# Performance work log

Hardware: AMD Instinct MI355X
Metric: run time of the kernel (lower is better)

Reference implementation:

```python
import jax, jax.numpy as jnp
import numpy as np

N_NODES = 100000


def _mean_agg(x, src, dst, n_nodes):
    # gather neighbor (src) features, segment-sum into destination nodes, divide by in-degree
    summed = jax.ops.segment_sum(x[src], dst, num_segments=n_nodes)  # [N, d]
    deg = jax.ops.segment_sum(jnp.ones_like(dst, dtype=x.dtype), dst, num_segments=n_nodes)
    return summed / jnp.clip(deg, 1.0)[:, None]  # DGL clamps zero in-degree to 1


def _sage_conv(x, src, dst, W_self, W_neigh, b, n_nodes):
    h_neigh = _mean_agg(x, src, dst, n_nodes)
    # DGL SAGEConv(mean): fc_self(h_self) + fc_neigh(h_neigh); single bias
    return x @ W_self + h_neigh @ W_neigh + b


def setup_inputs() -> dict:
    key = jax.random.key(0)
    ks = jax.random.split(key, 8)
    in_f, hid_f, out_f = 64, 64, 16
    n_edges = 1200000
    return {
        "x": jax.random.normal(ks[0], (N_NODES, in_f), dtype=jnp.float32),
        "src": jax.random.randint(ks[1], (n_edges,), 0, N_NODES),
        "dst": jax.random.randint(ks[2], (n_edges,), 0, N_NODES),
        "W1_self": jax.random.normal(ks[3], (in_f, hid_f), dtype=jnp.float32) / np.sqrt(in_f),
        "W1_neigh": jax.random.normal(ks[4], (in_f, hid_f), dtype=jnp.float32) / np.sqrt(in_f),
        "b1": jnp.zeros((hid_f,), dtype=jnp.float32),
        "W2_self": jax.random.normal(ks[5], (hid_f, out_f), dtype=jnp.float32) / np.sqrt(hid_f),
        "W2_neigh": jax.random.normal(ks[6], (hid_f, out_f), dtype=jnp.float32) / np.sqrt(hid_f),
        "b2": jnp.zeros((out_f,), dtype=jnp.float32),
    }


def reference(x, src, dst, W1_self, W1_neigh, b1, W2_self, W2_neigh, b2):
    h = _sage_conv(x, src, dst, W1_self, W1_neigh, b1, N_NODES)
    h = jax.nn.relu(h)
    h = _sage_conv(h, src, dst, W2_self, W2_neigh, b2, N_NODES)
    return h
```

## Files before the change

### kernel.cpp

```cpp
#include <hip/hip_runtime.h>

#define N_NODES 100000
#define N_EDGES 1200000
#define BK 64
#define NB 1563
#define CHUNK_E 4096
#define NBLK_E 293
#define TOT_H (NB * NBLK_E)
#define NSB2 ((TOT_H + 1023) / 1024)
#define CAP 1536
#define ND1 3125

#define OFF_ROWPTR 0
#define OFF_HISTG  401408
#define OFF_BLK2   2234368
#define OFF_PAIRS  2236416
#define OFF_SORTED 7036928
#define OFF_Y1     11837440
#define OFF_H1     24637440

__device__ __forceinline__ unsigned short f2bf(float f) {
    unsigned u = __float_as_uint(f);
    unsigned r = (u + 0x7fffu + ((u >> 16) & 1u)) >> 16;
    return (unsigned short)r;
}

__global__ __launch_bounds__(256) void hist_dense1_kernel(
    const int* __restrict__ dst, int* __restrict__ hist_g,
    const float* __restrict__ x,
    const float* __restrict__ Wn, const float* __restrict__ Ws,
    const float* __restrict__ b,
    unsigned short* __restrict__ y1, float* __restrict__ z1)
{
    __shared__ float sx[32 * 64];
    const int t = threadIdx.x;

    if (blockIdx.x < NBLK_E) {
        int* h = (int*)sx;
        const int e0 = blockIdx.x * CHUNK_E;
        const int e1 = min(e0 + CHUNK_E, N_EDGES);
        for (int i = t; i < NB; i += 256) h[i] = 0;
        __syncthreads();
        for (int e = e0 + t; e < e1; e += 256)
            atomicAdd(&h[dst[e] >> 6], 1);
        __syncthreads();
        for (int i = t; i < NB; i += 256)
            hist_g[i * NBLK_E + blockIdx.x] = h[i];
        return;
    }

    const int bid = blockIdx.x - NBLK_E;
    const int w = t >> 6;
    const int lane = t & 63;
    const int half = w >> 1;
    const int nsub = (w & 1) * 16;
    const int chunk = bid * 32;

    {
        const float4* gx = (const float4*)(x + (size_t)chunk * 64);
        float4* sx4 = (float4*)sx;
        sx4[t] = gx[t];
        sx4[t + 256] = gx[t + 256];
    }

    const float* W = half ? Ws : Wn;
    float wr[64];
#pragma unroll
    for (int k = 0; k < 64; ++k) wr[k] = W[k * 64 + lane];
    const float bj = half ? b[lane] : 0.f;

    __syncthreads();

#pragma unroll 2
    for (int m = 0; m < 16; ++m) {
        const int node = nsub + m;
        const float4* xr = (const float4*)(sx + node * 64);
        float a0 = 0.f, a1 = 0.f, a2 = 0.f, a3 = 0.f;
#pragma unroll
        for (int k4 = 0; k4 < 16; ++k4) {
            float4 v = xr[k4];
            a0 += v.x * wr[4 * k4 + 0];
            a1 += v.y * wr[4 * k4 + 1];
            a2 += v.z * wr[4 * k4 + 2];
            a3 += v.w * wr[4 * k4 + 3];
        }
        const float o = (a0 + a1) + (a2 + a3) + bj;
        const size_t gn = (size_t)(chunk + node);
        if (half) z1[gn * 64 + lane] = o;
        else      y1[gn * 64 + lane] = f2bf(o);
    }
}

__global__ __launch_bounds__(1024) void scan2_blocks_kernel(
    int* __restrict__ hist_g, int* __restrict__ blk2)
{
    __shared__ int wsum[16];
    const int t = threadIdx.x;
    const int i = blockIdx.x * 1024 + t;
    const int v = (i < TOT_H) ? hist_g[i] : 0;
    int inc = v;
#pragma unroll
    for (int off = 1; off < 64; off <<= 1) {
        int n = __shfl_up(inc, off);
        if ((t & 63) >= off) inc += n;
    }
    const int wid = t >> 6;
    if ((t & 63) == 63) wsum[wid] = inc;
    __syncthreads();
    if (t < 16) {
        int s = wsum[t];
#pragma unroll
        for (int off = 1; off < 16; off <<= 1) {
            int n = __shfl_up(s, off);
            if (t >= off) s += n;
        }
        wsum[t] = s;
    }
    __syncthreads();
    const int base = (wid > 0) ? wsum[wid - 1] : 0;
    const int incl = inc + base;
    if (i < TOT_H) hist_g[i] = incl - v;
    if (t == 1023) blk2[blockIdx.x] = incl;
}

__global__ __launch_bounds__(512) void tops_scan_kernel(int* __restrict__ blk2)
{
    __shared__ int wsum[8];
    const int t = threadIdx.x;
    const int v = (t < NSB2) ? blk2[t] : 0;
    int inc = v;
#pragma unroll
    for (int off = 1; off < 64; off <<= 1) {
        int n = __shfl_up(inc, off);
        if ((t & 63) >= off) inc += n;
    }
    const int wid = t >> 6;
    if ((t & 63) == 63) wsum[wid] = inc;
    __syncthreads();
    if (t < 8) {
        int s = wsum[t];
#pragma unroll
        for (int off = 1; off < 8; off <<= 1) {
            int n = __shfl_up(s, off);
            if (t >= off) s += n;
        }
        wsum[t] = s;
    }
    __syncthreads();
    const int base = (wid > 0) ? wsum[wid - 1] : 0;
    if (t < NSB2) blk2[t] = inc + base - v;
}

__global__ __launch_bounds__(512) void pair_scatter_kernel(
    const int* __restrict__ src, const int* __restrict__ dst,
    const int* __restrict__ hs_scan, const int* __restrict__ blk2,
    unsigned* __restrict__ pairs)
{
    __shared__ int base_s[NB];
    __shared__ int cur_s[NB];
    const int b = blockIdx.x;
    const int t = threadIdx.x;
    const int e0 = b * CHUNK_E;
    const int e1 = min(e0 + CHUNK_E, N_EDGES);

    for (int i = t; i < NB; i += 512) {
        int idx = i * NBLK_E + b;
        base_s[i] = hs_scan[idx] + blk2[idx >> 10];
        cur_s[i] = 0;
    }
    __syncthreads();
    for (int e = e0 + t; e < e1; e += 512) {
        int d = dst[e];
        int bk = d >> 6;
        int pos = base_s[bk] + atomicAdd(&cur_s[bk], 1);
        pairs[pos] = ((unsigned)src[e] << 6) | (unsigned)(d & 63);
    }
}

__global__ __launch_bounds__(512) void fused_gather1_kernel(
    const unsigned short* __restrict__ y1,
    const unsigned* __restrict__ pairs,
    const int* __restrict__ hs_scan, const int* __restrict__ blk2,
    int* __restrict__ row_ptr, int* __restrict__ sorted_src,
    float* __restrict__ h1)
{
    __shared__ int slist[CAP];
    __shared__ int hist[BK];
    __shared__ int sc[BK];
    __shared__ int cur[BK];
    const int b = blockIdx.x;
    const int t = threadIdx.x;

    const int i0 = b * NBLK_E;
    const int start = hs_scan[i0] + blk2[i0 >> 10];
    const int end = (b == NB - 1) ? N_EDGES
                    : hs_scan[i0 + NBLK_E] + blk2[(i0 + NBLK_E) >> 10];
    const int cnt = end - start;
    const int node0 = b * BK;

    if (t < BK) hist[t] = 0;
    __syncthreads();
    for (int e = start + t; e < end; e += 512)
        atomicAdd(&hist[pairs[e] & 63u], 1);
    __syncthreads();

    int v = 0;
    if (t < BK) {
        v = hist[t];
        int inc = v;
#pragma unroll
        for (int off = 1; off < 64; off <<= 1) {
            int n = __shfl_up(inc, off);
            if (t >= off) inc += n;
        }
        sc[t] = inc;
    }
    __syncthreads();
    const int excl = (t < BK) ? sc[t] - v : 0;
    if (t < BK && node0 + t < N_NODES) row_ptr[node0 + t] = start + excl;
    if (b == NB - 1 && t == 0) row_ptr[N_NODES] = N_EDGES;
    if (t < BK) cur[t] = excl;
    __syncthreads();

    const int wv = t >> 6;
    const int lane = t & 63;
    const int sub = lane >> 5;
    const int sl = lane & 31;
    const int eg = sl >> 3;
    const int fl = sl & 7;

    if (cnt <= CAP) {
        for (int e = start + t; e < end; e += 512) {
            unsigned u = pairs[e];
            int p = atomicAdd(&cur[u & 63u], 1);
            slist[p] = (int)(u >> 6);
        }
        __syncthreads();
        for (int i = t; i < cnt; i += 512)
            sorted_src[start + i] = slist[i];
#pragma unroll 2
        for (int q = 0; q < 4; ++q) {
            const int node = wv * 8 + q * 2 + sub;
            const int gn = node0 + node;
            if (gn < N_NODES) {
            const int o = sc[node] - hist[node];
            const int dg = hist[node];
            float4* hp = (float4*)(h1 + (size_t)gn * 64);
            float4 z;
            if (eg < 2) z = hp[fl * 2 + eg];
            float a0 = 0.f, a1 = 0.f, a2 = 0.f, a3 = 0.f;
            float a4 = 0.f, a5 = 0.f, a6 = 0.f, a7 = 0.f;
            for (int base = 0; base < dg; base += 8) {
                const int i0e = base + eg;
                const int i1e = base + 4 + eg;
                const bool v0 = i0e < dg, v1 = i1e < dg;
                uint4 r0, r1;
                if (v0) {
                    const int s = slist[o + i0e];
                    r0 = ((const uint4*)(y1 + (size_t)s * 64))[fl];
                }
                if (v1) {
                    const int s = slist[o + i1e];
                    r1 = ((const uint4*)(y1 + (size_t)s * 64))[fl];
                }
                if (v0) {
                    a0 += __uint_as_float(r0.x << 16);
                    a1 += __uint_as_float(r0.x & 0xffff0000u);
                    a2 += __uint_as_float(r0.y << 16);
                    a3 += __uint_as_float(r0.y & 0xffff0000u);
                    a4 += __uint_as_float(r0.z << 16);
                    a5 += __uint_as_float(r0.z & 0xffff0000u);
                    a6 += __uint_as_float(r0.w << 16);
                    a7 += __uint_as_float(r0.w & 0xffff0000u);
                }
                if (v1) {
                    a0 += __uint_as_float(r1.x << 16);
                    a1 += __uint_as_float(r1.x & 0xffff0000u);
                    a2 += __uint_as_float(r1.y << 16);
                    a3 += __uint_as_float(r1.y & 0xffff0000u);
                    a4 += __uint_as_float(r1.z << 16);
                    a5 += __uint_as_float(r1.z & 0xffff0000u);
                    a6 += __uint_as_float(r1.w << 16);
                    a7 += __uint_as_float(r1.w & 0xffff0000u);
                }
            }
#pragma unroll
            for (int d = 8; d <= 16; d <<= 1) {
                a0 += __shfl_xor(a0, d); a1 += __shfl_xor(a1, d);
                a2 += __shfl_xor(a2, d); a3 += __shfl_xor(a3, d);
                a4 += __shfl_xor(a4, d); a5 += __shfl_xor(a5, d);
                a6 += __shfl_xor(a6, d); a7 += __shfl_xor(a7, d);
            }
            const float invd = 1.0f / (float)max(dg, 1);
            if (eg == 0) {
                hp[fl * 2] = make_float4(fmaxf(z.x + a0 * invd, 0.f),
                                         fmaxf(z.y + a1 * invd, 0.f),
                                         fmaxf(z.z + a2 * invd, 0.f),
                                         fmaxf(z.w + a3 * invd, 0.f));
            } else if (eg == 1) {
                hp[fl * 2 + 1] = make_float4(fmaxf(z.x + a4 * invd, 0.f),
                                             fmaxf(z.y + a5 * invd, 0.f),
                                             fmaxf(z.z + a6 * invd, 0.f),
                                             fmaxf(z.w + a7 * invd, 0.f));
            }
            }
        }
    } else {
        if (t < BK) cur[t] = start + excl;
        __syncthreads();
        for (int e = start + t; e < end; e += 512) {
            unsigned u = pairs[e];
            int p = atomicAdd(&cur[u & 63u], 1);
            sorted_src[p] = (int)(u >> 6);
        }
        __syncthreads();
        for (int q = 0; q < 4; ++q) {
            const int node = wv * 8 + q * 2 + sub;
            const int gn = node0 + node;
            if (gn < N_NODES) {
            const int o = start + sc[node] - hist[node];
            const int dg = hist[node];
            float4* hp = (float4*)(h1 + (size_t)gn * 64);
            float4 z;
            if (eg < 2) z = hp[fl * 2 + eg];
            float a0 = 0.f, a1 = 0.f, a2 = 0.f, a3 = 0.f;
            float a4 = 0.f, a5 = 0.f, a6 = 0.f, a7 = 0.f;
            for (int base = 0; base < dg; base += 4) {
                const int idx = base + eg;
                if (idx < dg) {
                    const int s = sorted_src[o + idx];
                    uint4 raw = ((const uint4*)(y1 + (size_t)s * 64))[fl];
                    a0 += __uint_as_float(raw.x << 16);
                    a1 += __uint_as_float(raw.x & 0xffff0000u);
                    a2 += __uint_as_float(raw.y << 16);
                    a3 += __uint_as_float(raw.y & 0xffff0000u);
                    a4 += __uint_as_float(raw.z << 16);
                    a5 += __uint_as_float(raw.z & 0xffff0000u);
                    a6 += __uint_as_float(raw.w << 16);
                    a7 += __uint_as_float(raw.w & 0xffff0000u);
                }
            }
#pragma unroll
            for (int d = 8; d <= 16; d <<= 1) {
                a0 += __shfl_xor(a0, d); a1 += __shfl_xor(a1, d);
                a2 += __shfl_xor(a2, d); a3 += __shfl_xor(a3, d);
                a4 += __shfl_xor(a4, d); a5 += __shfl_xor(a5, d);
                a6 += __shfl_xor(a6, d); a7 += __shfl_xor(a7, d);
            }
            const float invd = 1.0f / (float)max(dg, 1);
            if (eg == 0) {
                hp[fl * 2] = make_float4(fmaxf(z.x + a0 * invd, 0.f),
                                         fmaxf(z.y + a1 * invd, 0.f),
                                         fmaxf(z.z + a2 * invd, 0.f),
                                         fmaxf(z.w + a3 * invd, 0.f));
            } else if (eg == 1) {
                hp[fl * 2 + 1] = make_float4(fmaxf(z.x + a4 * invd, 0.f),
                                             fmaxf(z.y + a5 * invd, 0.f),
                                             fmaxf(z.z + a6 * invd, 0.f),
                                             fmaxf(z.w + a7 * invd, 0.f));
            }
            }
        }
    }
}

__global__ __launch_bounds__(256) void dense2_kernel(
    const float* __restrict__ h1,
    const float* __restrict__ Wn, const float* __restrict__ Ws,
    const float* __restrict__ b,
    float* __restrict__ y2, float* __restrict__ out)
{
    __shared__ float sx[32 * 68];
    const int t = threadIdx.x;
    const int w = t >> 6;
    const int lane = t & 63;
    const int half = w >> 1;
    const int nsub = (w & 1) * 16;
    const int j = lane & 15;
    const int g = lane >> 4;
    const int chunk = blockIdx.x * 32;

    {
        const float4* gx = (const float4*)(h1 + (size_t)chunk * 64);
        float4* sx4 = (float4*)sx;
        int r0 = t >> 4, c0 = t & 15;
        sx4[r0 * 17 + c0] = gx[t];
        sx4[(r0 + 16) * 17 + c0] = gx[t + 256];
    }

    const float* W = half ? Ws : Wn;
    float wr[64];
#pragma unroll
    for (int k = 0; k < 64; ++k) wr[k] = W[k * 16 + j];
    const float bj = half ? b[j] : 0.f;

    __syncthreads();

#pragma unroll 2
    for (int q = 0; q < 4; ++q) {
        const int node = nsub + q * 4 + g;
        const float4* xr = (const float4*)(sx + node * 68);
        float a0 = 0.f, a1 = 0.f, a2 = 0.f, a3 = 0.f;
#pragma unroll
        for (int k4 = 0; k4 < 16; ++k4) {
            float4 v = xr[k4];
            a0 += v.x * wr[4 * k4 + 0];
            a1 += v.y * wr[4 * k4 + 1];
            a2 += v.z * wr[4 * k4 + 2];
            a3 += v.w * wr[4 * k4 + 3];
        }
        const float o = (a0 + a1) + (a2 + a3) + bj;
        const size_t gn = (size_t)(chunk + node);
        if (half) out[gn * 16 + j] = o;
        else      y2[gn * 16 + j] = o;
    }
}

__global__ __launch_bounds__(256) void gather2_kernel(
    const float* __restrict__ y2,
    const int* __restrict__ row_ptr,
    const int* __restrict__ sorted_src,
    float* __restrict__ out)
{
    const int wv = threadIdx.x >> 6;
    const int lane = threadIdx.x & 63;
    const int sub = lane >> 4;
    const int sl = lane & 15;
    const int eg = sl >> 2;
    const int fl = sl & 3;

    const int n = blockIdx.x * 16 + wv * 4 + sub;
    const int start = row_ptr[n];
    const int deg = row_ptr[n + 1] - start;

    float4* op = (float4*)(out + (size_t)n * 16);
    float4 z;
    if (eg == 0) z = op[fl];

    float4 acc = make_float4(0.f, 0.f, 0.f, 0.f);
    for (int base = 0; base < deg; base += 16) {
        int eid = 0;
        if (base + sl < deg) eid = sorted_src[start + base + sl];
#pragma unroll
        for (int jj = 0; jj < 16; jj += 4) {
            const int idx = jj + eg;
            const int s = __shfl(eid, sub * 16 + idx);
            if (base + idx < deg) {
                float4 v = ((const float4*)(y2 + (size_t)s * 16))[fl];
                acc.x += v.x; acc.y += v.y; acc.z += v.z; acc.w += v.w;
            }
        }
    }
#pragma unroll
    for (int d = 4; d <= 8; d <<= 1) {
        acc.x += __shfl_xor(acc.x, d); acc.y += __shfl_xor(acc.y, d);
        acc.z += __shfl_xor(acc.z, d); acc.w += __shfl_xor(acc.w, d);
    }
    const float invd = 1.0f / (float)max(deg, 1);
    if (eg == 0) {
        op[fl] = make_float4(z.x + acc.x * invd, z.y + acc.y * invd,
                             z.z + acc.z * invd, z.w + acc.w * invd);
    }
}

extern "C" void kernel_launch(void* const* d_in, const int* in_sizes, int n_in,
                              void* d_out, int out_size, void* d_ws, size_t ws_size,
                              hipStream_t stream) {
    const float* x   = (const float*)d_in[0];
    const int*   src = (const int*)d_in[1];
    const int*   dst = (const int*)d_in[2];
    const float* W1s = (const float*)d_in[3];
    const float* W1n = (const float*)d_in[4];
    const float* b1  = (const float*)d_in[5];
    const float* W2s = (const float*)d_in[6];
    const float* W2n = (const float*)d_in[7];
    const float* b2  = (const float*)d_in[8];
    float* out = (float*)d_out;

    char* ws = (char*)d_ws;
    int* row_ptr    = (int*)(ws + OFF_ROWPTR);
    int* hist_g     = (int*)(ws + OFF_HISTG);
    int* blk2       = (int*)(ws + OFF_BLK2);
    unsigned* pairs = (unsigned*)(ws + OFF_PAIRS);
    int* sorted_src = (int*)(ws + OFF_SORTED);
    unsigned short* y1 = (unsigned short*)(ws + OFF_Y1);
    float* y2       = (float*)(ws + OFF_Y1);
    float* h1       = (float*)(ws + OFF_H1);

    hist_dense1_kernel<<<NBLK_E + ND1, 256, 0, stream>>>(
        dst, hist_g, x, W1n, W1s, b1, y1, h1);
    scan2_blocks_kernel<<<NSB2, 1024, 0, stream>>>(hist_g, blk2);
    tops_scan_kernel<<<1, 512, 0, stream>>>(blk2);
    pair_scatter_kernel<<<NBLK_E, 512, 0, stream>>>(src, dst, hist_g, blk2, pairs);
    fused_gather1_kernel<<<NB, 512, 0, stream>>>(y1, pairs, hist_g, blk2,
                                                 row_ptr, sorted_src, h1);
    dense2_kernel<<<ND1, 256, 0, stream>>>(h1, W2n, W2s, b2, y2, out);
    gather2_kernel<<<N_NODES / 16, 256, 0, stream>>>(y2, row_ptr, sorted_src, out);
}
```

Before: 210.0 us.

## Replace two-level bucketed CSR build with per-node degree count and atomic scatter

Builds the CSR with one global per-node degree histogram (global atomics), a flat scan over 100k nodes, and a scatter that places src directly using global per-node atomic cursors. This drops the 64-node bucket histogram, the pairs buffer and the in-block LDS sort in the gather kernel. Gather kernels now compute row ranges from the scanned degrees plus block offsets. The cost is heavy contention on global atomics and a memset, and neighbor order within each row becomes nondeterministic, so float summation order varies between runs.

```diff
diff --git a/kernel.cpp b/kernel.cpp
--- a/kernel.cpp
+++ b/kernel.cpp
@@ -6,18 +6,15 @@
 #define NB 1563
 #define CHUNK_E 4096
 #define NBLK_E 293
-#define TOT_H (NB * NBLK_E)
-#define NSB2 ((TOT_H + 1023) / 1024)
-#define CAP 1536
+#define NSB 98
 #define ND1 3125
 
-#define OFF_ROWPTR 0
-#define OFF_HISTG  401408
-#define OFF_BLK2   2234368
-#define OFF_PAIRS  2236416
-#define OFF_SORTED 7036928
-#define OFF_Y1     11837440
-#define OFF_H1     24637440
+#define OFF_DEG    0
+#define OFF_CNT    400000
+#define OFF_BLK2   800000
+#define OFF_SORTED 801024
+#define OFF_Y1     5601024
+#define OFF_H1     18401024
 
 __device__ __forceinline__ unsigned short f2bf(float f) {
     unsigned u = __float_as_uint(f);
@@ -26,7 +23,7 @@
 }
 
 __global__ __launch_bounds__(256) void hist_dense1_kernel(
-    const int* __restrict__ dst, int* __restrict__ hist_g,
+    const int* __restrict__ dst, int* __restrict__ deg,
     const float* __restrict__ x,
     const float* __restrict__ Wn, const float* __restrict__ Ws,
     const float* __restrict__ b,
@@ -36,16 +33,10 @@
     const int t = threadIdx.x;
 
     if (blockIdx.x < NBLK_E) {
-        int* h = (int*)sx;
         const int e0 = blockIdx.x * CHUNK_E;
         const int e1 = min(e0 + CHUNK_E, N_EDGES);
-        for (int i = t; i < NB; i += 256) h[i] = 0;
-        __syncthreads();
         for (int e = e0 + t; e < e1; e += 256)
-            atomicAdd(&h[dst[e] >> 6], 1);
-        __syncthreads();
-        for (int i = t; i < NB; i += 256)
-            hist_g[i * NBLK_E + blockIdx.x] = h[i];
+            atomicAdd(&deg[dst[e]], 1);
         return;
     }
 
@@ -91,13 +82,13 @@
     }
 }
 
-__global__ __launch_bounds__(1024) void scan2_blocks_kernel(
-    int* __restrict__ hist_g, int* __restrict__ blk2)
+__global__ __launch_bounds__(1024) void scan_deg_kernel(
+    int* __restrict__ deg, int* __restrict__ blk2)
 {
     __shared__ int wsum[16];
     const int t = threadIdx.x;
     const int i = blockIdx.x * 1024 + t;
-    const int v = (i < TOT_H) ? hist_g[i] : 0;
+    const int v = (i < N_NODES) ? deg[i] : 0;
     int inc = v;
 #pragma unroll
     for (int off = 1; off < 64; off <<= 1) {
@@ -119,7 +110,7 @@
     __syncthreads();
     const int base = (wid > 0) ? wsum[wid - 1] : 0;
     const int incl = inc + base;
-    if (i < TOT_H) hist_g[i] = incl - v;
+    if (i < N_NODES) deg[i] = incl - v;
     if (t == 1023) blk2[blockIdx.x] = incl;
 }
 
@@ -127,7 +118,7 @@
 {
     __shared__ int wsum[8];
     const int t = threadIdx.x;
-    const int v = (t < NSB2) ? blk2[t] : 0;
+    const int v = (t < NSB) ? blk2[t] : 0;
     int inc = v;
 #pragma unroll
     for (int off = 1; off < 64; off <<= 1) {
@@ -148,79 +139,33 @@
     }
     __syncthreads();
     const int base = (wid > 0) ? wsum[wid - 1] : 0;
-    if (t < NSB2) blk2[t] = inc + base - v;
-}
-
-__global__ __launch_bounds__(512) void pair_scatter_kernel(
+    if (t < NSB) blk2[t] = inc + base - v;
+}
+
+__global__ __launch_bounds__(512) void scatter_kernel(
     const int* __restrict__ src, const int* __restrict__ dst,
-    const int* __restrict__ hs_scan, const int* __restrict__ blk2,
-    unsigned* __restrict__ pairs)
-{
-    __shared__ int base_s[NB];
-    __shared__ int cur_s[NB];
+    const int* __restrict__ dscan, const int* __restrict__ blk2,
+    int* __restrict__ cnt, int* __restrict__ sorted_src)
+{
+    const int e0 = blockIdx.x * CHUNK_E;
+    const int e1 = min(e0 + CHUNK_E, N_EDGES);
+    for (int e = e0 + threadIdx.x; e < e1; e += 512) {
+        const int d = dst[e];
+        const int base = dscan[d] + blk2[d >> 10];
+        const int pos = base + atomicAdd(&cnt[d], 1);
+        sorted_src[pos] = src[e];
+    }
+}
+
+__global__ __launch_bounds__(512) void gather1_kernel(
+    const unsigned short* __restrict__ y1,
+    const int* __restrict__ dscan, const int* __restrict__ blk2,
+    const int* __restrict__ sorted_src,
+    float* __restrict__ h1)
+{
     const int b = blockIdx.x;
     const int t = threadIdx.x;
-    const int e0 = b * CHUNK_E;
-    const int e1 = min(e0 + CHUNK_E, N_EDGES);
-
-    for (int i = t; i < NB; i += 512) {
-        int idx = i * NBLK_E + b;
-        base_s[i] = hs_scan[idx] + blk2[idx >> 10];
-        cur_s[i] = 0;
-    }
-    __syncthreads();
-    for (int e = e0 + t; e < e1; e += 512) {
-        int d = dst[e];
-        int bk = d >> 6;
-        int pos = base_s[bk] + atomicAdd(&cur_s[bk], 1);
-        pairs[pos] = ((unsigned)src[e] << 6) | (unsigned)(d & 63);
-    }
-}
-
-__global__ __launch_bounds__(512) void fused_gather1_kernel(
-    const unsigned short* __restrict__ y1,
-    const unsigned* __restrict__ pairs,
-    const int* __restrict__ hs_scan, const int* __restrict__ blk2,
-    int* __restrict__ row_ptr, int* __restrict__ sorted_src,
-    float* __restrict__ h1)
-{
-    __shared__ int slist[CAP];
-    __shared__ int hist[BK];
-    __shared__ int sc[BK];
-    __shared__ int cur[BK];
-    const int b = blockIdx.x;
-    const int t = threadIdx.x;
-
-    const int i0 = b * NBLK_E;
-    const int start = hs_scan[i0] + blk2[i0 >> 10];
-    const int end = (b == NB - 1) ? N_EDGES
-                    : hs_scan[i0 + NBLK_E] + blk2[(i0 + NBLK_E) >> 10];
-    const int cnt = end - start;
     const int node0 = b * BK;
-
-    if (t < BK) hist[t] = 0;
-    __syncthreads();
-    for (int e = start + t; e < end; e += 512)
-        atomicAdd(&hist[pairs[e] & 63u], 1);
-    __syncthreads();
-
-    int v = 0;
-    if (t < BK) {
-        v = hist[t];
-        int inc = v;
-#pragma unroll
-        for (int off = 1; off < 64; off <<= 1) {
-            int n = __shfl_up(inc, off);
-            if (t >= off) inc += n;
-        }
-        sc[t] = inc;
-    }
-    __syncthreads();
-    const int excl = (t < BK) ? sc[t] - v : 0;
-    if (t < BK && node0 + t < N_NODES) row_ptr[node0 + t] = start + excl;
-    if (b == NB - 1 && t == 0) row_ptr[N_NODES] = N_EDGES;
-    if (t < BK) cur[t] = excl;
-    __syncthreads();
 
     const int wv = t >> 6;
     const int lane = t & 63;
@@ -229,137 +174,73 @@
     const int eg = sl >> 3;
     const int fl = sl & 7;
 
-    if (cnt <= CAP) {
-        for (int e = start + t; e < end; e += 512) {
-            unsigned u = pairs[e];
-            int p = atomicAdd(&cur[u & 63u], 1);
-            slist[p] = (int)(u >> 6);
-        }
-        __syncthreads();
-        for (int i = t; i < cnt; i += 512)
-            sorted_src[start + i] = slist[i];
 #pragma unroll 2
-        for (int q = 0; q < 4; ++q) {
-            const int node = wv * 8 + q * 2 + sub;
-            const int gn = node0 + node;
-            if (gn < N_NODES) {
-            const int o = sc[node] - hist[node];
-            const int dg = hist[node];
-            float4* hp = (float4*)(h1 + (size_t)gn * 64);
-            float4 z;
-            if (eg < 2) z = hp[fl * 2 + eg];
-            float a0 = 0.f, a1 = 0.f, a2 = 0.f, a3 = 0.f;
-            float a4 = 0.f, a5 = 0.f, a6 = 0.f, a7 = 0.f;
-            for (int base = 0; base < dg; base += 8) {
-                const int i0e = base + eg;
-                const int i1e = base + 4 + eg;
-                const bool v0 = i0e < dg, v1 = i1e < dg;
-                uint4 r0, r1;
-                if (v0) {
-                    const int s = slist[o + i0e];
-                    r0 = ((const uint4*)(y1 + (size_t)s * 64))[fl];
-                }
-                if (v1) {
-                    const int s = slist[o + i1e];
-                    r1 = ((const uint4*)(y1 + (size_t)s * 64))[fl];
-                }
-                if (v0) {
-                    a0 += __uint_as_float(r0.x << 16);
-                    a1 += __uint_as_float(r0.x & 0xffff0000u);
-                    a2 += __uint_as_float(r0.y << 16);
-                    a3 += __uint_as_float(r0.y & 0xffff0000u);
-                    a4 += __uint_as_float(r0.z << 16);
-                    a5 += __uint_as_float(r0.z & 0xffff0000u);
-                    a6 += __uint_as_float(r0.w << 16);
-                    a7 += __uint_as_float(r0.w & 0xffff0000u);
-                }
-                if (v1) {
-                    a0 += __uint_as_float(r1.x << 16);
-                    a1 += __uint_as_float(r1.x & 0xffff0000u);
-                    a2 += __uint_as_float(r1.y << 16);
-                    a3 += __uint_as_float(r1.y & 0xffff0000u);
-                    a4 += __uint_as_float(r1.z << 16);
-                    a5 += __uint_as_float(r1.z & 0xffff0000u);
-                    a6 += __uint_as_float(r1.w << 16);
-                    a7 += __uint_as_float(r1.w & 0xffff0000u);
-                }
-            }
-#pragma unroll
-            for (int d = 8; d <= 16; d <<= 1) {
-                a0 += __shfl_xor(a0, d); a1 += __shfl_xor(a1, d);
-                a2 += __shfl_xor(a2, d); a3 += __shfl_xor(a3, d);
-                a4 += __shfl_xor(a4, d); a5 += __shfl_xor(a5, d);
-                a6 += __shfl_xor(a6, d); a7 += __shfl_xor(a7, d);
-            }
-            const float invd = 1.0f / (float)max(dg, 1);
-            if (eg == 0) {
-                hp[fl * 2] = make_float4(fmaxf(z.x + a0 * invd, 0.f),
-                                         fmaxf(z.y + a1 * invd, 0.f),
-                                         fmaxf(z.z + a2 * invd, 0.f),
-                                         fmaxf(z.w + a3 * invd, 0.f));
-            } else if (eg == 1) {
-                hp[fl * 2 + 1] = make_float4(fmaxf(z.x + a4 * invd, 0.f),
-                                             fmaxf(z.y + a5 * invd, 0.f),
-                                             fmaxf(z.z + a6 * invd, 0.f),
-                                             fmaxf(z.w + a7 * invd, 0.f));
-            }
-            }
-        }
-    } else {
-        if (t < BK) cur[t] = start + excl;
-        __syncthreads();
-        for (int e = start + t; e < end; e += 512) {
-            unsigned u = pairs[e];
-            int p = atomicAdd(&cur[u & 63u], 1);
-            sorted_src[p] = (int)(u >> 6);
-        }
-        __syncthreads();
-        for (int q = 0; q < 4; ++q) {
-            const int node = wv * 8 + q * 2 + sub;
-            const int gn = node0 + node;
-            if (gn < N_NODES) {
-            const int o = start + sc[node] - hist[node];
-            const int dg = hist[node];
-            float4* hp = (float4*)(h1 + (size_t)gn * 64);
-            float4 z;
-            if (eg < 2) z = hp[fl * 2 + eg];
-            float a0 = 0.f, a1 = 0.f, a2 = 0.f, a3 = 0.f;
-            float a4 = 0.f, a5 = 0.f, a6 = 0.f, a7 = 0.f;
-            for (int base = 0; base < dg; base += 4) {
-                const int idx = base + eg;
-                if (idx < dg) {
-                    const int s = sorted_src[o + idx];
-                    uint4 raw = ((const uint4*)(y1 + (size_t)s * 64))[fl];
-                    a0 += __uint_as_float(raw.x << 16);
-                    a1 += __uint_as_float(raw.x & 0xffff0000u);
-                    a2 += __uint_as_float(raw.y << 16);
-                    a3 += __uint_as_float(raw.y & 0xffff0000u);
-                    a4 += __uint_as_float(raw.z << 16);
-                    a5 += __uint_as_float(raw.z & 0xffff0000u);
-                    a6 += __uint_as_float(raw.w << 16);
-                    a7 += __uint_as_float(raw.w & 0xffff0000u);
-                }
-            }
-#pragma unroll
-            for (int d = 8; d <= 16; d <<= 1) {
-                a0 += __shfl_xor(a0, d); a1 += __shfl_xor(a1, d);
-                a2 += __shfl_xor(a2, d); a3 += __shfl_xor(a3, d);
-                a4 += __shfl_xor(a4, d); a5 += __shfl_xor(a5, d);
-                a6 += __shfl_xor(a6, d); a7 += __shfl_xor(a7, d);
-            }
-            const float invd = 1.0f / (float)max(dg, 1);
-            if (eg == 0) {
-                hp[fl * 2] = make_float4(fmaxf(z.x + a0 * invd, 0.f),
-                                         fmaxf(z.y + a1 * invd, 0.f),
-                                         fmaxf(z.z + a2 * invd, 0.f),
-                                         fmaxf(z.w + a3 * invd, 0.f));
-            } else if (eg == 1) {
-                hp[fl * 2 + 1] = make_float4(fmaxf(z.x + a4 * invd, 0.f),
-                                             fmaxf(z.y + a5 * invd, 0.f),
-                                             fmaxf(z.z + a6 * invd, 0.f),
-                                             fmaxf(z.w + a7 * invd, 0.f));
-            }
-            }
+    for (int q = 0; q < 4; ++q) {
+        const int node = wv * 8 + q * 2 + sub;
+        const int gn = node0 + node;
+        if (gn < N_NODES) {
+        const int start = dscan[gn] + blk2[gn >> 10];
+        const int end = (gn + 1 < N_NODES)
+                        ? dscan[gn + 1] + blk2[(gn + 1) >> 10] : N_EDGES;
+        const int dg = end - start;
+        float4* hp = (float4*)(h1 + (size_t)gn * 64);
+        float4 z;
+        if (eg < 2) z = hp[fl * 2 + eg];
+        float a0 = 0.f, a1 = 0.f, a2 = 0.f, a3 = 0.f;
+        float a4 = 0.f, a5 = 0.f, a6 = 0.f, a7 = 0.f;
+        for (int base = 0; base < dg; base += 8) {
+            const int i0e = base + eg;
+            const int i1e = base + 4 + eg;
+            const bool v0 = i0e < dg, v1 = i1e < dg;
+            uint4 r0, r1;
+            if (v0) {
+                const int s = sorted_src[start + i0e];
+                r0 = ((const uint4*)(y1 + (size_t)s * 64))[fl];
+            }
+            if (v1) {
+                const int s = sorted_src[start + i1e];
+                r1 = ((const uint4*)(y1 + (size_t)s * 64))[fl];
+            }
+            if (v0) {
+                a0 += __uint_as_float(r0.x << 16);
+                a1 += __uint_as_float(r0.x & 0xffff0000u);
+                a2 += __uint_as_float(r0.y << 16);
+                a3 += __uint_as_float(r0.y & 0xffff0000u);
+                a4 += __uint_as_float(r0.z << 16);
+                a5 += __uint_as_float(r0.z & 0xffff0000u);
+                a6 += __uint_as_float(r0.w << 16);
+                a7 += __uint_as_float(r0.w & 0xffff0000u);
+            }
+            if (v1) {
+                a0 += __uint_as_float(r1.x << 16);
+                a1 += __uint_as_float(r1.x & 0xffff0000u);
+                a2 += __uint_as_float(r1.y << 16);
+                a3 += __uint_as_float(r1.y & 0xffff0000u);
+                a4 += __uint_as_float(r1.z << 16);
+                a5 += __uint_as_float(r1.z & 0xffff0000u);
+                a6 += __uint_as_float(r1.w << 16);
+                a7 += __uint_as_float(r1.w & 0xffff0000u);
+            }
+        }
+#pragma unroll
+        for (int d = 8; d <= 16; d <<= 1) {
+            a0 += __shfl_xor(a0, d); a1 += __shfl_xor(a1, d);
+            a2 += __shfl_xor(a2, d); a3 += __shfl_xor(a3, d);
+            a4 += __shfl_xor(a4, d); a5 += __shfl_xor(a5, d);
+            a6 += __shfl_xor(a6, d); a7 += __shfl_xor(a7, d);
+        }
+        const float invd = 1.0f / (float)max(dg, 1);
+        if (eg == 0) {
+            hp[fl * 2] = make_float4(fmaxf(z.x + a0 * invd, 0.f),
+                                     fmaxf(z.y + a1 * invd, 0.f),
+                                     fmaxf(z.z + a2 * invd, 0.f),
+                                     fmaxf(z.w + a3 * invd, 0.f));
+        } else if (eg == 1) {
+            hp[fl * 2 + 1] = make_float4(fmaxf(z.x + a4 * invd, 0.f),
+                                         fmaxf(z.y + a5 * invd, 0.f),
+                                         fmaxf(z.z + a6 * invd, 0.f),
+                                         fmaxf(z.w + a7 * invd, 0.f));
+        }
         }
     }
 }
@@ -418,7 +299,7 @@
 
 __global__ __launch_bounds__(256) void gather2_kernel(
     const float* __restrict__ y2,
-    const int* __restrict__ row_ptr,
+    const int* __restrict__ dscan, const int* __restrict__ blk2,
     const int* __restrict__ sorted_src,
     float* __restrict__ out)
 {
@@ -430,8 +311,10 @@
     const int fl = sl & 3;
 
     const int n = blockIdx.x * 16 + wv * 4 + sub;
-    const int start = row_ptr[n];
-    const int deg = row_ptr[n + 1] - start;
+    const int start = dscan[n] + blk2[n >> 10];
+    const int end = (n + 1 < N_NODES)
+                    ? dscan[n + 1] + blk2[(n + 1) >> 10] : N_EDGES;
+    const int deg = end - start;
 
     float4* op = (float4*)(out + (size_t)n * 16);
     float4 z;
@@ -478,22 +361,21 @@
     float* out = (float*)d_out;
 
     char* ws = (char*)d_ws;
-    int* row_ptr    = (int*)(ws + OFF_ROWPTR);
-    int* hist_g     = (int*)(ws + OFF_HISTG);
+    int* deg        = (int*)(ws + OFF_DEG);
+    int* cnt        = (int*)(ws + OFF_CNT);
     int* blk2       = (int*)(ws + OFF_BLK2);
-    unsigned* pairs = (unsigned*)(ws + OFF_PAIRS);
     int* sorted_src = (int*)(ws + OFF_SORTED);
     unsigned short* y1 = (unsigned short*)(ws + OFF_Y1);
     float* y2       = (float*)(ws + OFF_Y1);
     float* h1       = (float*)(ws + OFF_H1);
 
+    hipMemsetAsync(ws + OFF_DEG, 0, 800000, stream);
     hist_dense1_kernel<<<NBLK_E + ND1, 256, 0, stream>>>(
-        dst, hist_g, x, W1n, W1s, b1, y1, h1);
-    scan2_blocks_kernel<<<NSB2, 1024, 0, stream>>>(hist_g, blk2);
+        dst, deg, x, W1n, W1s, b1, y1, h1);
+    scan_deg_kernel<<<NSB, 1024, 0, stream>>>(deg, blk2);
     tops_scan_kernel<<<1, 512, 0, stream>>>(blk2);
-    pair_scatter_kernel<<<NBLK_E, 512, 0, stream>>>(src, dst, hist_g, blk2, pairs);
-    fused_gather1_kernel<<<NB, 512, 0, stream>>>(y1, pairs, hist_g, blk2,
-                                                 row_ptr, sorted_src, h1);
+    scatter_kernel<<<NBLK_E, 512, 0, stream>>>(src, dst, deg, blk2, cnt, sorted_src);
+    gather1_kernel<<<NB, 512, 0, stream>>>(y1, deg, blk2, sorted_src, h1);
     dense2_kernel<<<ND1, 256, 0, stream>>>(h1, W2n, W2s, b2, y2, out);
-    gather2_kernel<<<N_NODES / 16, 256, 0, stream>>>(y2, row_ptr, sorted_src, out);
-}
+    gather2_kernel<<<N_NODES / 16, 256, 0, stream>>>(y2, deg, blk2, sorted_src, out);
+}
```

New measurement: 301.4 us. +43.5%, slower.
